# Performance work log

Measured on AMD Instinct MI355X. Metric: run time of the kernel, lower is better.

## Reference

```python
import jax, jax.numpy as jnp
import numpy as np

K = 20          # neighbors
BN_EPS = 1e-5


def _knn_idx(x, k):
    """x: [B, C, N] -> idx of k nearest neighbors [B, N, k] (by squared distance, self included)."""
    xx = jnp.sum(x * x, axis=1)                       # [B, N]
    inner = jnp.einsum('bcn,bcm->bnm', x, x)          # [B, N, N]
    neg_sqdist = 2.0 * inner - xx[:, :, None] - xx[:, None, :]
    return jax.lax.top_k(neg_sqdist, k)[1]            # [B, N, k]


def _graph_feature(x, k):
    """x: [B, C, N] -> edge features cat(x_j - x_i, x_i): [B, 2C, N, k]."""
    idx = _knn_idx(x, k)                              # [B, N, k]
    xT = x.transpose(0, 2, 1)                         # [B, N, C]
    nbrs = jax.vmap(lambda xt, ii: xt[ii])(xT, idx)   # [B, N, k, C] gather
    center = xT[:, :, None, :]                        # [B, N, 1, C]
    feat = jnp.concatenate(
        [nbrs - center, jnp.broadcast_to(center, nbrs.shape)], axis=-1)  # [B, N, k, 2C]
    return feat.transpose(0, 3, 1, 2)                 # [B, 2C, N, k]


def _conv_bn_lrelu(feat, W, gamma, beta, mean, var):
    """1x1 Conv2d (no bias) + BatchNorm (given stats) + LeakyReLU(0.2). feat: [B, Cin, N, k]."""
    y = jnp.einsum('oc,bcnk->bonk', W, feat)
    scale = (gamma / jnp.sqrt(var + BN_EPS))[None, :, None, None]
    y = (y - mean[None, :, None, None]) * scale + beta[None, :, None, None]
    return jnp.where(y > 0, y, 0.2 * y)


def setup_inputs() -> dict:
    key = jax.random.key(0)
    ks = list(jax.random.split(key, 32))
    B, N = 8, 1024
    f32 = jnp.float32

    def w(kk, o, i):
        return jax.random.normal(kk, (o, i), dtype=f32) / np.sqrt(i)

    def bn(k1, k2, k3, k4, c):
        g = jax.random.uniform(k1, (c,), dtype=f32, minval=0.5, maxval=1.5)
        b = jax.random.normal(k2, (c,), dtype=f32) * 0.05
        m = jax.random.normal(k3, (c,), dtype=f32) * 0.05
        v = jax.random.uniform(k4, (c,), dtype=f32, minval=0.5, maxval=1.5)
        return g, b, m, v

    x = jax.random.normal(ks[0], (B, N, 3), dtype=f32)
    W0 = w(ks[1], 64, 6);    g0, b0, m0, v0 = bn(ks[2], ks[3], ks[4], ks[5], 64)
    W1 = w(ks[6], 128, 128); g1, b1, m1, v1 = bn(ks[7], ks[8], ks[9], ks[10], 128)
    W2 = w(ks[11], 256, 256); g2, b2, m2, v2 = bn(ks[12], ks[13], ks[14], ks[15], 256)
    Wf = w(ks[16], 512, 896); gf, bf, mf, vf = bn(ks[17], ks[18], ks[19], ks[20], 512)
    We = w(ks[21], 256, 512)
    return dict(x=x,
                W0=W0, g0=g0, b0=b0, m0=m0, v0=v0,
                W1=W1, g1=g1, b1=b1, m1=m1, v1=v1,
                W2=W2, g2=g2, b2=b2, m2=m2, v2=v2,
                Wf=Wf, gf=gf, bf=bf, mf=mf, vf=vf,
                We=We)


def reference(x, W0, g0, b0, m0, v0, W1, g1, b1, m1, v1,
              W2, g2, b2, m2, v2, Wf, gf, bf, mf, vf, We):
    h = x.transpose(0, 2, 1)                          # [B, 3, N]
    outs = []
    for (W, g, b, m, v) in ((W0, g0, b0, m0, v0),
                            (W1, g1, b1, m1, v1),
                            (W2, g2, b2, m2, v2)):
        gfeat = _graph_feature(h, K)                  # [B, 2C, N, k]
        y = _conv_bn_lrelu(gfeat, W, g, b, m, v)      # [B, Cout, N, k]
        h = y.mean(axis=-1)                           # max-free EdgeConv pool over k
        outs.append(h)
    cat = jnp.concatenate(outs, axis=1)               # [B, 448, N]
    gfeat = _graph_feature(cat, K)                    # [B, 896, N, k]
    y = _conv_bn_lrelu(gfeat, Wf, gf, bf, mf, vf)     # [B, 512, N, k]
    pooled = y.mean(axis=-1).mean(axis=-1)            # [B, 512] (pool over k then N)
    return pooled @ We.T                              # [B, num_features]
```

## Files before the change

### kernel.cpp

```cpp
#include <hip/hip_runtime.h>
#include <cstdint>

#define KNN 20
#define BV 8
#define NV 1024

template <int CTRL>
__device__ __forceinline__ unsigned dppmax(unsigned x) {
    unsigned m = (unsigned)__builtin_amdgcn_update_dpp((int)x, (int)x, CTRL, 0xf, 0xf, false);
    return (x > m) ? x : m;
}
template <int CTRL>
__device__ __forceinline__ unsigned dppmin(unsigned x) {
    unsigned m = (unsigned)__builtin_amdgcn_update_dpp((int)x, (int)x, CTRL, 0xf, 0xf, false);
    return (x < m) ? x : m;
}
__device__ __forceinline__ unsigned wave_max_u32(unsigned x) {
    x = dppmax<0xB1>(x); x = dppmax<0x4E>(x); x = dppmax<0x141>(x);
    x = dppmax<0x140>(x); x = dppmax<0x142>(x); x = dppmax<0x143>(x);
    return (unsigned)__builtin_amdgcn_readlane((int)x, 63);
}
__device__ __forceinline__ unsigned wave_min_u32(unsigned x) {
    x = dppmin<0xB1>(x); x = dppmin<0x4E>(x); x = dppmin<0x141>(x);
    x = dppmin<0x140>(x); x = dppmin<0x142>(x); x = dppmin<0x143>(x);
    return (unsigned)__builtin_amdgcn_readlane((int)x, 63);
}

__global__ __launch_bounds__(256) void k_transpose(const float* __restrict__ x, float* __restrict__ hx) {
    int id = blockIdx.x * 256 + threadIdx.x;
    if (id >= BV * 3 * NV) return;
    int n = id % NV;
    int c = (id / NV) % 3;
    int b = id / (3 * NV);
    hx[id] = x[(b * NV + n) * 3 + c];
}

__global__ __launch_bounds__(256) void k_xx(const float* __restrict__ h, float* __restrict__ xx,
                                            int C, int bstride) {
    int id = blockIdx.x * 256 + threadIdx.x;
    int n = id % NV, b = id / NV;
    if (b >= BV) return;
    const float* hp = h + (size_t)b * bstride + n;
    float s = 0.f;
    for (int c = 0; c < C; ++c) { float v = hp[(size_t)c * NV]; s += v * v; }
    xx[b * NV + n] = s;
}

__global__ __launch_bounds__(512, 4) void k_knn(const float* __restrict__ h, const float* __restrict__ xx,
                                                int C, int bstride, int* __restrict__ idx) {
    __shared__ float Bs[8][1024];
    const int bx = blockIdx.x;
    const int b = bx & 7, tile = bx >> 3;
    const int i0 = tile * 16;
    const int t = threadIdx.x, lane = t & 63, w = t >> 6;
    const int irow = i0 + w * 2;
    float acc[2][16] = {};
    const float* hb = h + (size_t)b * bstride;

    for (int c0 = 0; c0 < C; c0 += 8) {
        __syncthreads();
#pragma unroll
        for (int r = 0; r < 4; ++r) {
            int e = r * 512 + t;
            int cc = e >> 8, jj = e & 255;
            float4 v = make_float4(0.f, 0.f, 0.f, 0.f);
            if (c0 + cc < C) v = *(const float4*)&hb[(size_t)(c0 + cc) * NV + jj * 4];
            *(float4*)&Bs[cc][jj * 4] = v;
        }
        __syncthreads();
#pragma unroll
        for (int c = 0; c < 8; ++c) {
            float2 arv = *(const float2*)&Bs[c][irow];
            float ar[2] = {arv.x, arv.y};
            float br[16];
#pragma unroll
            for (int g = 0; g < 4; ++g) {
                float4 bv = *(const float4*)&Bs[c][g * 256 + (lane << 2)];
                br[g * 4 + 0] = bv.x; br[g * 4 + 1] = bv.y;
                br[g * 4 + 2] = bv.z; br[g * 4 + 3] = bv.w;
            }
#pragma unroll
            for (int a = 0; a < 2; ++a)
#pragma unroll
                for (int q = 0; q < 16; ++q) acc[a][q] += ar[a] * br[q];
        }
    }

    const float* xb = xx + b * NV;
    float xxj[16];
#pragma unroll
    for (int g = 0; g < 4; ++g) {
        float4 xv = *(const float4*)&xb[g * 256 + (lane << 2)];
        xxj[g * 4 + 0] = xv.x; xxj[g * 4 + 1] = xv.y;
        xxj[g * 4 + 2] = xv.z; xxj[g * 4 + 3] = xv.w;
    }
    unsigned ua[2][16];
#pragma unroll
    for (int a = 0; a < 2; ++a) {
        float xi = xb[irow + a];
#pragma unroll
        for (int q = 0; q < 16; ++q) {
            float d = 2.f * acc[a][q] - xi - xxj[q];
            unsigned u = __float_as_uint(d);
            ua[a][q] = ((int)u < 0) ? ~u : (u | 0x80000000u);
        }
    }

    int* opb = idx + ((size_t)(b * NV + irow)) * KNN;
#pragma unroll 1
    for (int s = 0; s < KNN; ++s) {
#pragma unroll
        for (int a = 0; a < 2; ++a) {
            unsigned w0[8]; int p0[8];
#pragma unroll
            for (int i = 0; i < 8; ++i) {
                bool g = ua[a][2 * i + 1] > ua[a][2 * i];
                w0[i] = g ? ua[a][2 * i + 1] : ua[a][2 * i];
                p0[i] = g ? 2 * i + 1 : 2 * i;
            }
            unsigned w1[4]; int p1[4];
#pragma unroll
            for (int i = 0; i < 4; ++i) {
                bool g = w1[0], gg = w0[2 * i + 1] > w0[2 * i];
                (void)g;
                w1[i] = gg ? w0[2 * i + 1] : w0[2 * i];
                p1[i] = gg ? p0[2 * i + 1] : p0[2 * i];
            }
            unsigned w2[2]; int p2[2];
#pragma unroll
            for (int i = 0; i < 2; ++i) {
                bool gg = w1[2 * i + 1] > w1[2 * i];
                w2[i] = gg ? w1[2 * i + 1] : w1[2 * i];
                p2[i] = gg ? p1[2 * i + 1] : p1[2 * i];
            }
            bool gf = w2[1] > w2[0];
            unsigned su = gf ? w2[1] : w2[0];
            int bq = gf ? p2[1] : p2[0];

            unsigned gmax = wave_max_u32(su);
            int myj = ((bq >> 2) << 8) + (lane << 2) + (bq & 3);
            unsigned cand = (su == gmax) ? (unsigned)myj : 0xFFFFFFFFu;
            int j = (int)wave_min_u32(cand);
            if (lane == 0) opb[a * KNN + s] = j;
            int wq = (cand == (unsigned)j) ? bq : 99;
#pragma unroll
            for (int q = 0; q < 16; ++q)
                if (wq == q) ua[a][q] = 0u;
        }
    }
}

__global__ __launch_bounds__(256) void k_pack(const float* __restrict__ W, float* __restrict__ wb,
                                              int C, int O) {
    int id = blockIdx.x * 256 + threadIdx.x;
    if (id >= 2 * O * C) return;
    int c = id % C, o = (id / C) % O, half = id / (C * O);
    float wl = W[(size_t)o * 2 * C + c];
    wb[id] = half ? (W[(size_t)o * 2 * C + C + c] - wl) : wl;
}

__global__ __launch_bounds__(256) void k_gemm(const float* __restrict__ A, int astride,
                                              const float* __restrict__ h, int bstride, int C,
                                              float* __restrict__ out, int O) {
    __shared__ float Ws[8][64], Hs[8][128];
    const int b = blockIdx.x, n0 = blockIdx.y * 128, o0 = blockIdx.z * 64;
    const int t = threadIdx.x, tx = t & 15, ty = t >> 4;
    float acc[4][8] = {};
    const float* hb = h + (size_t)b * bstride;
    for (int c0 = 0; c0 < C; c0 += 8) {
#pragma unroll
        for (int q = 0; q < 2; ++q) {
            int e = t + q * 256;
            int oo = e >> 3, cc = e & 7;
            Ws[cc][oo] = ((c0 + cc) < C) ? A[(size_t)(o0 + oo) * astride + c0 + cc] : 0.f;
        }
        {
            int cc = t >> 5, nn4 = t & 31;
            float4 v = make_float4(0.f, 0.f, 0.f, 0.f);
            if (c0 + cc < C) v = *(const float4*)&hb[(size_t)(c0 + cc) * NV + n0 + nn4 * 4];
            *(float4*)&Hs[cc][nn4 * 4] = v;
        }
        __syncthreads();
#pragma unroll
        for (int c = 0; c < 8; ++c) {
            float4 wv = *(const float4*)&Ws[c][ty * 4];
            float ar[4] = {wv.x, wv.y, wv.z, wv.w};
            float br[8];
            float4 h0 = *(const float4*)&Hs[c][tx * 4];
            float4 h1 = *(const float4*)&Hs[c][64 + tx * 4];
            br[0] = h0.x; br[1] = h0.y; br[2] = h0.z; br[3] = h0.w;
            br[4] = h1.x; br[5] = h1.y; br[6] = h1.z; br[7] = h1.w;
#pragma unroll
            for (int a = 0; a < 4; ++a)
#pragma unroll
                for (int q = 0; q < 8; ++q) acc[a][q] += ar[a] * br[q];
        }
        __syncthreads();
    }
#pragma unroll
    for (int a = 0; a < 4; ++a) {
        int o = o0 + ty * 4 + a;
        float* outp = out + ((size_t)b * O + o) * NV + n0;
        float4 s0 = make_float4(acc[a][0], acc[a][1], acc[a][2], acc[a][3]);
        float4 s1 = make_float4(acc[a][4], acc[a][5], acc[a][6], acc[a][7]);
        *(float4*)&outp[tx * 4] = s0;
        *(float4*)&outp[64 + tx * 4] = s1;
    }
}

__global__ __launch_bounds__(256) void k_edge(const float* __restrict__ pd,
                                              const int* __restrict__ idx,
                                              const float* __restrict__ ga, const float* __restrict__ be,
                                              const float* __restrict__ mu, const float* __restrict__ va,
                                              float* __restrict__ out, int out_bstride, int O) {
    const int b = blockIdx.x;
    const int n = blockIdx.y * 256 + threadIdx.x;
    const int o0 = blockIdx.z * 4;
    const int* ip = idx + ((size_t)b * NV + n) * KNN;
    int jj[KNN];
#pragma unroll
    for (int k = 0; k < KNN; ++k) jj[k] = ip[k];
#pragma unroll
    for (int a = 0; a < 4; ++a) {
        const int o = o0 + a;
        const float al = ga[o] / sqrtf(va[o] + 1e-5f);
        const float c0 = be[o] - mu[o] * al;
        const float* pb = pd + ((size_t)b * 2 * O + o) * NV;
        const float dv  = pd[((size_t)b * 2 * O + O + o) * NV + n];
        float s = 0.f;
#pragma unroll
        for (int k = 0; k < KNN; ++k) {
            float y = fmaf(al, pb[jj[k]] + dv, c0);
            s += (y > 0.f) ? y : 0.2f * y;
        }
        out[(size_t)b * out_bstride + (size_t)o * NV + n] = s * (1.f / KNN);
    }
}

__global__ __launch_bounds__(256) void k_pool(const float* __restrict__ hf, float* __restrict__ pooled) {
    const int o = blockIdx.x, b = blockIdx.y;
    const float* hp = hf + ((size_t)b * 512 + o) * NV;
    float s = 0.f;
    for (int i = threadIdx.x; i < NV; i += 256) s += hp[i];
#pragma unroll
    for (int off = 32; off > 0; off >>= 1) s += __shfl_down(s, off, 64);
    __shared__ float red[4];
    if ((threadIdx.x & 63) == 0) red[threadIdx.x >> 6] = s;
    __syncthreads();
    if (threadIdx.x == 0)
        pooled[(size_t)b * 512 + o] = (red[0] + red[1] + red[2] + red[3]) * (1.f / NV);
}

__global__ __launch_bounds__(256) void k_final(const float* __restrict__ pooled, const float* __restrict__ We,
                                               float* __restrict__ out) {
    const int j = threadIdx.x, b = blockIdx.x;
    __shared__ float ps[512];
    for (int o = threadIdx.x; o < 512; o += 256) ps[o] = pooled[b * 512 + o];
    __syncthreads();
    float s = 0.f;
    for (int o = 0; o < 512; ++o) s += ps[o] * We[(size_t)j * 512 + o];
    out[b * 256 + j] = s;
}

extern "C" void kernel_launch(void* const* d_in, const int* in_sizes, int n_in,
                              void* d_out, int out_size, void* d_ws, size_t ws_size,
                              hipStream_t stream) {
    const float* x  = (const float*)d_in[0];
    const float* W0 = (const float*)d_in[1];
    const float* g0 = (const float*)d_in[2];
    const float* b0 = (const float*)d_in[3];
    const float* m0 = (const float*)d_in[4];
    const float* v0 = (const float*)d_in[5];
    const float* W1 = (const float*)d_in[6];
    const float* g1 = (const float*)d_in[7];
    const float* b1 = (const float*)d_in[8];
    const float* m1 = (const float*)d_in[9];
    const float* v1 = (const float*)d_in[10];
    const float* W2 = (const float*)d_in[11];
    const float* g2 = (const float*)d_in[12];
    const float* b2 = (const float*)d_in[13];
    const float* m2 = (const float*)d_in[14];
    const float* v2 = (const float*)d_in[15];
    const float* Wf = (const float*)d_in[16];
    const float* gf = (const float*)d_in[17];
    const float* bf = (const float*)d_in[18];
    const float* mf = (const float*)d_in[19];
    const float* vf = (const float*)d_in[20];
    const float* We = (const float*)d_in[21];

    float* ws = (float*)d_ws;
    float* hx     = ws;
    float* cat    = hx + 24576;
    float* xx     = cat + 3670016;
    int*   idx    = (int*)(xx + 8192);
    float* pd     = (float*)(idx + 163840);
    float* wb     = pd + 8388608;
    float* hf     = wb + 458752;
    float* pooled = hf + 4194304;

    k_transpose<<<96, 256, 0, stream>>>(x, hx);

    auto run_layer = [&](const float* h, int C, int bstride, const float* W,
                         const float* g, const float* be, const float* m, const float* v,
                         int O, float* outp, int obstride) {
        k_xx<<<32, 256, 0, stream>>>(h, xx, C, bstride);
        k_knn<<<512, 512, 0, stream>>>(h, xx, C, bstride, idx);
        int pn = 2 * O * C;
        k_pack<<<(pn + 255) / 256, 256, 0, stream>>>(W, wb, C, O);
        k_gemm<<<dim3(8, 8, 2 * O / 64), 256, 0, stream>>>(wb, C, h, bstride, C, pd, 2 * O);
        k_edge<<<dim3(8, 4, O / 4), 256, 0, stream>>>(pd, idx, g, be, m, v, outp, obstride, O);
    };

    run_layer(hx, 3, 3 * NV, W0, g0, b0, m0, v0, 64, cat, 448 * NV);
    run_layer(cat, 64, 448 * NV, W1, g1, b1, m1, v1, 128, cat + 64 * NV, 448 * NV);
    run_layer(cat + 64 * NV, 128, 448 * NV, W2, g2, b2, m2, v2, 256, cat + 192 * NV, 448 * NV);
    run_layer(cat, 448, 448 * NV, Wf, gf, bf, mf, vf, 512, hf, 512 * NV);

    k_pool<<<dim3(512, 8), 256, 0, stream>>>(hf, pooled);
    k_final<<<8, 256, 0, stream>>>(pooled, We, (float*)d_out);
}
```

Baseline: 802.6 us.

## Enlarge kNN and GEMM register tiles, prefetch kNN loads, use float top-k compare

The kNN kernel now computes 4 query rows per wave instead of 2, which halves the block count. It also prefetches the next 8-channel slab into registers while computing the current one, and runs the top-k selection directly on float distances with a float DPP max instead of an order-preserving uint transform. The edge GEMM tile grows from 64x128 to 128x128 with an 8x8 register tile per thread. The aim is more arithmetic reuse per shared-memory load and hidden global-load latency, at the cost of higher register pressure and fewer blocks for occupancy.

```diff
diff --git a/kernel.cpp b/kernel.cpp
--- a/kernel.cpp
+++ b/kernel.cpp
@@ -6,19 +6,20 @@
 #define NV 1024
 
 template <int CTRL>
-__device__ __forceinline__ unsigned dppmax(unsigned x) {
-    unsigned m = (unsigned)__builtin_amdgcn_update_dpp((int)x, (int)x, CTRL, 0xf, 0xf, false);
-    return (x > m) ? x : m;
+__device__ __forceinline__ float dppmaxf(float x) {
+    int xi = __float_as_int(x);
+    int mi = __builtin_amdgcn_update_dpp(xi, xi, CTRL, 0xf, 0xf, false);
+    return fmaxf(x, __int_as_float(mi));
 }
 template <int CTRL>
 __device__ __forceinline__ unsigned dppmin(unsigned x) {
     unsigned m = (unsigned)__builtin_amdgcn_update_dpp((int)x, (int)x, CTRL, 0xf, 0xf, false);
     return (x < m) ? x : m;
 }
-__device__ __forceinline__ unsigned wave_max_u32(unsigned x) {
-    x = dppmax<0xB1>(x); x = dppmax<0x4E>(x); x = dppmax<0x141>(x);
-    x = dppmax<0x140>(x); x = dppmax<0x142>(x); x = dppmax<0x143>(x);
-    return (unsigned)__builtin_amdgcn_readlane((int)x, 63);
+__device__ __forceinline__ float wave_max_f32(float x) {
+    x = dppmaxf<0xB1>(x); x = dppmaxf<0x4E>(x); x = dppmaxf<0x141>(x);
+    x = dppmaxf<0x140>(x); x = dppmaxf<0x142>(x); x = dppmaxf<0x143>(x);
+    return __int_as_float(__builtin_amdgcn_readlane(__float_as_int(x), 63));
 }
 __device__ __forceinline__ unsigned wave_min_u32(unsigned x) {
     x = dppmin<0xB1>(x); x = dppmin<0x4E>(x); x = dppmin<0x141>(x);
@@ -46,32 +47,45 @@
     xx[b * NV + n] = s;
 }
 
-__global__ __launch_bounds__(512, 4) void k_knn(const float* __restrict__ h, const float* __restrict__ xx,
+__global__ __launch_bounds__(512, 2) void k_knn(const float* __restrict__ h, const float* __restrict__ xx,
                                                 int C, int bstride, int* __restrict__ idx) {
     __shared__ float Bs[8][1024];
     const int bx = blockIdx.x;
     const int b = bx & 7, tile = bx >> 3;
-    const int i0 = tile * 16;
+    const int i0 = tile * 32;
     const int t = threadIdx.x, lane = t & 63, w = t >> 6;
-    const int irow = i0 + w * 2;
-    float acc[2][16] = {};
+    const int irow = i0 + w * 4;
+    float acc[4][16] = {};
     const float* hb = h + (size_t)b * bstride;
+
+    int cc_[4], jj_[4];
+#pragma unroll
+    for (int r = 0; r < 4; ++r) { int e = r * 512 + t; cc_[r] = e >> 8; jj_[r] = (e & 255) * 4; }
+
+    float4 pf[4];
+#pragma unroll
+    for (int r = 0; r < 4; ++r) {
+        pf[r] = make_float4(0.f, 0.f, 0.f, 0.f);
+        if (cc_[r] < C) pf[r] = *(const float4*)&hb[(size_t)cc_[r] * NV + jj_[r]];
+    }
 
     for (int c0 = 0; c0 < C; c0 += 8) {
         __syncthreads();
 #pragma unroll
-        for (int r = 0; r < 4; ++r) {
-            int e = r * 512 + t;
-            int cc = e >> 8, jj = e & 255;
-            float4 v = make_float4(0.f, 0.f, 0.f, 0.f);
-            if (c0 + cc < C) v = *(const float4*)&hb[(size_t)(c0 + cc) * NV + jj * 4];
-            *(float4*)&Bs[cc][jj * 4] = v;
-        }
+        for (int r = 0; r < 4; ++r) *(float4*)&Bs[cc_[r]][jj_[r]] = pf[r];
         __syncthreads();
+        int cn = c0 + 8;
+        if (cn < C) {
+#pragma unroll
+            for (int r = 0; r < 4; ++r) {
+                pf[r] = make_float4(0.f, 0.f, 0.f, 0.f);
+                if (cn + cc_[r] < C) pf[r] = *(const float4*)&hb[(size_t)(cn + cc_[r]) * NV + jj_[r]];
+            }
+        }
 #pragma unroll
         for (int c = 0; c < 8; ++c) {
-            float2 arv = *(const float2*)&Bs[c][irow];
-            float ar[2] = {arv.x, arv.y};
+            float4 arv = *(const float4*)&Bs[c][irow];
+            float ar[4] = {arv.x, arv.y, arv.z, arv.w};
             float br[16];
 #pragma unroll
             for (int g = 0; g < 4; ++g) {
@@ -80,7 +94,7 @@
                 br[g * 4 + 2] = bv.z; br[g * 4 + 3] = bv.w;
             }
 #pragma unroll
-            for (int a = 0; a < 2; ++a)
+            for (int a = 0; a < 4; ++a)
 #pragma unroll
                 for (int q = 0; q < 16; ++q) acc[a][q] += ar[a] * br[q];
         }
@@ -94,58 +108,52 @@
         xxj[g * 4 + 0] = xv.x; xxj[g * 4 + 1] = xv.y;
         xxj[g * 4 + 2] = xv.z; xxj[g * 4 + 3] = xv.w;
     }
-    unsigned ua[2][16];
-#pragma unroll
-    for (int a = 0; a < 2; ++a) {
+#pragma unroll
+    for (int a = 0; a < 4; ++a) {
         float xi = xb[irow + a];
 #pragma unroll
-        for (int q = 0; q < 16; ++q) {
-            float d = 2.f * acc[a][q] - xi - xxj[q];
-            unsigned u = __float_as_uint(d);
-            ua[a][q] = ((int)u < 0) ? ~u : (u | 0x80000000u);
-        }
+        for (int q = 0; q < 16; ++q) acc[a][q] = 2.f * acc[a][q] - xi - xxj[q];
     }
 
     int* opb = idx + ((size_t)(b * NV + irow)) * KNN;
 #pragma unroll 1
     for (int s = 0; s < KNN; ++s) {
 #pragma unroll
-        for (int a = 0; a < 2; ++a) {
-            unsigned w0[8]; int p0[8];
+        for (int a = 0; a < 4; ++a) {
+            float w0[8]; int p0[8];
 #pragma unroll
             for (int i = 0; i < 8; ++i) {
-                bool g = ua[a][2 * i + 1] > ua[a][2 * i];
-                w0[i] = g ? ua[a][2 * i + 1] : ua[a][2 * i];
+                bool g = acc[a][2 * i + 1] > acc[a][2 * i];
+                w0[i] = g ? acc[a][2 * i + 1] : acc[a][2 * i];
                 p0[i] = g ? 2 * i + 1 : 2 * i;
             }
-            unsigned w1[4]; int p1[4];
+            float w1[4]; int p1[4];
 #pragma unroll
             for (int i = 0; i < 4; ++i) {
-                bool g = w1[0], gg = w0[2 * i + 1] > w0[2 * i];
-                (void)g;
-                w1[i] = gg ? w0[2 * i + 1] : w0[2 * i];
-                p1[i] = gg ? p0[2 * i + 1] : p0[2 * i];
-            }
-            unsigned w2[2]; int p2[2];
+                bool g = w0[2 * i + 1] > w0[2 * i];
+                w1[i] = g ? w0[2 * i + 1] : w0[2 * i];
+                p1[i] = g ? p0[2 * i + 1] : p0[2 * i];
+            }
+            float w2[2]; int p2[2];
 #pragma unroll
             for (int i = 0; i < 2; ++i) {
-                bool gg = w1[2 * i + 1] > w1[2 * i];
-                w2[i] = gg ? w1[2 * i + 1] : w1[2 * i];
-                p2[i] = gg ? p1[2 * i + 1] : p1[2 * i];
+                bool g = w1[2 * i + 1] > w1[2 * i];
+                w2[i] = g ? w1[2 * i + 1] : w1[2 * i];
+                p2[i] = g ? p1[2 * i + 1] : p1[2 * i];
             }
             bool gf = w2[1] > w2[0];
-            unsigned su = gf ? w2[1] : w2[0];
+            float bv = gf ? w2[1] : w2[0];
             int bq = gf ? p2[1] : p2[0];
 
-            unsigned gmax = wave_max_u32(su);
+            float gmax = wave_max_f32(bv);
             int myj = ((bq >> 2) << 8) + (lane << 2) + (bq & 3);
-            unsigned cand = (su == gmax) ? (unsigned)myj : 0xFFFFFFFFu;
+            unsigned cand = (bv == gmax) ? (unsigned)myj : 0xFFFFFFFFu;
             int j = (int)wave_min_u32(cand);
             if (lane == 0) opb[a * KNN + s] = j;
             int wq = (cand == (unsigned)j) ? bq : 99;
 #pragma unroll
             for (int q = 0; q < 16; ++q)
-                if (wq == q) ua[a][q] = 0u;
+                if (wq == q) acc[a][q] = -3.4e38f;
         }
     }
 }
@@ -161,16 +169,16 @@
 
 __global__ __launch_bounds__(256) void k_gemm(const float* __restrict__ A, int astride,
                                               const float* __restrict__ h, int bstride, int C,
-                                              float* __restrict__ out, int O) {
-    __shared__ float Ws[8][64], Hs[8][128];
-    const int b = blockIdx.x, n0 = blockIdx.y * 128, o0 = blockIdx.z * 64;
+                                              float* __restrict__ out, int O2) {
+    __shared__ float Ws[8][128], Hs[8][128];
+    const int b = blockIdx.x, n0 = blockIdx.y * 128, o0 = blockIdx.z * 128;
     const int t = threadIdx.x, tx = t & 15, ty = t >> 4;
-    float acc[4][8] = {};
+    float acc[8][8] = {};
     const float* hb = h + (size_t)b * bstride;
     for (int c0 = 0; c0 < C; c0 += 8) {
 #pragma unroll
-        for (int q = 0; q < 2; ++q) {
-            int e = t + q * 256;
+        for (int k2 = 0; k2 < 4; ++k2) {
+            int e = t + k2 * 256;
             int oo = e >> 3, cc = e & 7;
             Ws[cc][oo] = ((c0 + cc) < C) ? A[(size_t)(o0 + oo) * astride + c0 + cc] : 0.f;
         }
@@ -183,28 +191,27 @@
         __syncthreads();
 #pragma unroll
         for (int c = 0; c < 8; ++c) {
-            float4 wv = *(const float4*)&Ws[c][ty * 4];
-            float ar[4] = {wv.x, wv.y, wv.z, wv.w};
-            float br[8];
-            float4 h0 = *(const float4*)&Hs[c][tx * 4];
-            float4 h1 = *(const float4*)&Hs[c][64 + tx * 4];
-            br[0] = h0.x; br[1] = h0.y; br[2] = h0.z; br[3] = h0.w;
-            br[4] = h1.x; br[5] = h1.y; br[6] = h1.z; br[7] = h1.w;
-#pragma unroll
-            for (int a = 0; a < 4; ++a)
+            float4 wv0 = *(const float4*)&Ws[c][ty * 8];
+            float4 wv1 = *(const float4*)&Ws[c][ty * 8 + 4];
+            float ar[8] = {wv0.x, wv0.y, wv0.z, wv0.w, wv1.x, wv1.y, wv1.z, wv1.w};
+            float4 h0 = *(const float4*)&Hs[c][tx * 8];
+            float4 h1 = *(const float4*)&Hs[c][tx * 8 + 4];
+            float br[8] = {h0.x, h0.y, h0.z, h0.w, h1.x, h1.y, h1.z, h1.w};
+#pragma unroll
+            for (int a = 0; a < 8; ++a)
 #pragma unroll
                 for (int q = 0; q < 8; ++q) acc[a][q] += ar[a] * br[q];
         }
         __syncthreads();
     }
 #pragma unroll
-    for (int a = 0; a < 4; ++a) {
-        int o = o0 + ty * 4 + a;
-        float* outp = out + ((size_t)b * O + o) * NV + n0;
+    for (int a = 0; a < 8; ++a) {
+        int o = o0 + ty * 8 + a;
+        float* outp = out + ((size_t)b * O2 + o) * NV + n0;
         float4 s0 = make_float4(acc[a][0], acc[a][1], acc[a][2], acc[a][3]);
         float4 s1 = make_float4(acc[a][4], acc[a][5], acc[a][6], acc[a][7]);
-        *(float4*)&outp[tx * 4] = s0;
-        *(float4*)&outp[64 + tx * 4] = s1;
+        *(float4*)&outp[tx * 8] = s0;
+        *(float4*)&outp[tx * 8 + 4] = s1;
     }
 }
 
@@ -304,10 +311,10 @@
                          const float* g, const float* be, const float* m, const float* v,
                          int O, float* outp, int obstride) {
         k_xx<<<32, 256, 0, stream>>>(h, xx, C, bstride);
-        k_knn<<<512, 512, 0, stream>>>(h, xx, C, bstride, idx);
+        k_knn<<<256, 512, 0, stream>>>(h, xx, C, bstride, idx);
         int pn = 2 * O * C;
         k_pack<<<(pn + 255) / 256, 256, 0, stream>>>(W, wb, C, O);
-        k_gemm<<<dim3(8, 8, 2 * O / 64), 256, 0, stream>>>(wb, C, h, bstride, C, pd, 2 * O);
+        k_gemm<<<dim3(8, 8, 2 * O / 128), 256, 0, stream>>>(wb, C, h, bstride, C, pd, 2 * O);
         k_edge<<<dim3(8, 4, O / 4), 256, 0, stream>>>(pd, idx, g, be, m, v, outp, obstride, O);
     };
 
```

After: 976.8 us. 21.7% more time.

## Fuse weight packing into GEMM, stage edge rows in LDS, float top-k selection

Applied to the files above, without the earlier changes.

Removes the separate k_pack launch by computing the packed weights (W_left and W_right - W_left) on the fly inside the GEMM tile load. Restructures k_edge so each block stages four output rows of the neighbor projection in shared memory and gathers neighbors from LDS instead of scattered global reads. The kNN selection now works directly on float scores with float DPP max instead of converting to order-preserving unsigned keys, and the kNN launch bound drops from 4 to 2 waves per SIMD so the compiler may use more registers. In exchange, the GEMM does slightly more global loads per tile, and taken entries are marked with a large negative float sentinel, which changes tie and NaN handling.

```diff
diff --git a/kernel.cpp b/kernel.cpp
--- a/kernel.cpp
+++ b/kernel.cpp
@@ -6,19 +6,20 @@
 #define NV 1024
 
 template <int CTRL>
-__device__ __forceinline__ unsigned dppmax(unsigned x) {
-    unsigned m = (unsigned)__builtin_amdgcn_update_dpp((int)x, (int)x, CTRL, 0xf, 0xf, false);
-    return (x > m) ? x : m;
+__device__ __forceinline__ float dppmaxf(float x) {
+    int xi = __float_as_int(x);
+    int mi = __builtin_amdgcn_update_dpp(xi, xi, CTRL, 0xf, 0xf, false);
+    return fmaxf(x, __int_as_float(mi));
 }
 template <int CTRL>
 __device__ __forceinline__ unsigned dppmin(unsigned x) {
     unsigned m = (unsigned)__builtin_amdgcn_update_dpp((int)x, (int)x, CTRL, 0xf, 0xf, false);
     return (x < m) ? x : m;
 }
-__device__ __forceinline__ unsigned wave_max_u32(unsigned x) {
-    x = dppmax<0xB1>(x); x = dppmax<0x4E>(x); x = dppmax<0x141>(x);
-    x = dppmax<0x140>(x); x = dppmax<0x142>(x); x = dppmax<0x143>(x);
-    return (unsigned)__builtin_amdgcn_readlane((int)x, 63);
+__device__ __forceinline__ float wave_max_f32(float x) {
+    x = dppmaxf<0xB1>(x); x = dppmaxf<0x4E>(x); x = dppmaxf<0x141>(x);
+    x = dppmaxf<0x140>(x); x = dppmaxf<0x142>(x); x = dppmaxf<0x143>(x);
+    return __int_as_float(__builtin_amdgcn_readlane(__float_as_int(x), 63));
 }
 __device__ __forceinline__ unsigned wave_min_u32(unsigned x) {
     x = dppmin<0xB1>(x); x = dppmin<0x4E>(x); x = dppmin<0x141>(x);
@@ -46,7 +47,7 @@
     xx[b * NV + n] = s;
 }
 
-__global__ __launch_bounds__(512, 4) void k_knn(const float* __restrict__ h, const float* __restrict__ xx,
+__global__ __launch_bounds__(512, 2) void k_knn(const float* __restrict__ h, const float* __restrict__ xx,
                                                 int C, int bstride, int* __restrict__ idx) {
     __shared__ float Bs[8][1024];
     const int bx = blockIdx.x;
@@ -94,16 +95,11 @@
         xxj[g * 4 + 0] = xv.x; xxj[g * 4 + 1] = xv.y;
         xxj[g * 4 + 2] = xv.z; xxj[g * 4 + 3] = xv.w;
     }
-    unsigned ua[2][16];
 #pragma unroll
     for (int a = 0; a < 2; ++a) {
         float xi = xb[irow + a];
 #pragma unroll
-        for (int q = 0; q < 16; ++q) {
-            float d = 2.f * acc[a][q] - xi - xxj[q];
-            unsigned u = __float_as_uint(d);
-            ua[a][q] = ((int)u < 0) ? ~u : (u | 0x80000000u);
-        }
+        for (int q = 0; q < 16; ++q) acc[a][q] = 2.f * acc[a][q] - xi - xxj[q];
     }
 
     int* opb = idx + ((size_t)(b * NV + irow)) * KNN;
@@ -111,57 +107,47 @@
     for (int s = 0; s < KNN; ++s) {
 #pragma unroll
         for (int a = 0; a < 2; ++a) {
-            unsigned w0[8]; int p0[8];
+            float w0[8]; int p0[8];
 #pragma unroll
             for (int i = 0; i < 8; ++i) {
-                bool g = ua[a][2 * i + 1] > ua[a][2 * i];
-                w0[i] = g ? ua[a][2 * i + 1] : ua[a][2 * i];
+                bool g = acc[a][2 * i + 1] > acc[a][2 * i];
+                w0[i] = g ? acc[a][2 * i + 1] : acc[a][2 * i];
                 p0[i] = g ? 2 * i + 1 : 2 * i;
             }
-            unsigned w1[4]; int p1[4];
+            float w1[4]; int p1[4];
 #pragma unroll
             for (int i = 0; i < 4; ++i) {
-                bool g = w1[0], gg = w0[2 * i + 1] > w0[2 * i];
-                (void)g;
-                w1[i] = gg ? w0[2 * i + 1] : w0[2 * i];
-                p1[i] = gg ? p0[2 * i + 1] : p0[2 * i];
-            }
-            unsigned w2[2]; int p2[2];
+                bool g = w0[2 * i + 1] > w0[2 * i];
+                w1[i] = g ? w0[2 * i + 1] : w0[2 * i];
+                p1[i] = g ? p0[2 * i + 1] : p0[2 * i];
+            }
+            float w2[2]; int p2[2];
 #pragma unroll
             for (int i = 0; i < 2; ++i) {
-                bool gg = w1[2 * i + 1] > w1[2 * i];
-                w2[i] = gg ? w1[2 * i + 1] : w1[2 * i];
-                p2[i] = gg ? p1[2 * i + 1] : p1[2 * i];
+                bool g = w1[2 * i + 1] > w1[2 * i];
+                w2[i] = g ? w1[2 * i + 1] : w1[2 * i];
+                p2[i] = g ? p1[2 * i + 1] : p1[2 * i];
             }
             bool gf = w2[1] > w2[0];
-            unsigned su = gf ? w2[1] : w2[0];
+            float bv = gf ? w2[1] : w2[0];
             int bq = gf ? p2[1] : p2[0];
 
-            unsigned gmax = wave_max_u32(su);
+            float gmax = wave_max_f32(bv);
             int myj = ((bq >> 2) << 8) + (lane << 2) + (bq & 3);
-            unsigned cand = (su == gmax) ? (unsigned)myj : 0xFFFFFFFFu;
+            unsigned cand = (bv == gmax) ? (unsigned)myj : 0xFFFFFFFFu;
             int j = (int)wave_min_u32(cand);
             if (lane == 0) opb[a * KNN + s] = j;
             int wq = (cand == (unsigned)j) ? bq : 99;
 #pragma unroll
             for (int q = 0; q < 16; ++q)
-                if (wq == q) ua[a][q] = 0u;
-        }
-    }
-}
-
-__global__ __launch_bounds__(256) void k_pack(const float* __restrict__ W, float* __restrict__ wb,
-                                              int C, int O) {
-    int id = blockIdx.x * 256 + threadIdx.x;
-    if (id >= 2 * O * C) return;
-    int c = id % C, o = (id / C) % O, half = id / (C * O);
-    float wl = W[(size_t)o * 2 * C + c];
-    wb[id] = half ? (W[(size_t)o * 2 * C + C + c] - wl) : wl;
-}
-
-__global__ __launch_bounds__(256) void k_gemm(const float* __restrict__ A, int astride,
+                if (wq == q) acc[a][q] = -3.4e38f;
+        }
+    }
+}
+
+__global__ __launch_bounds__(256) void k_gemm(const float* __restrict__ W, int O,
                                               const float* __restrict__ h, int bstride, int C,
-                                              float* __restrict__ out, int O) {
+                                              float* __restrict__ out) {
     __shared__ float Ws[8][64], Hs[8][128];
     const int b = blockIdx.x, n0 = blockIdx.y * 128, o0 = blockIdx.z * 64;
     const int t = threadIdx.x, tx = t & 15, ty = t >> 4;
@@ -172,7 +158,17 @@
         for (int q = 0; q < 2; ++q) {
             int e = t + q * 256;
             int oo = e >> 3, cc = e & 7;
-            Ws[cc][oo] = ((c0 + cc) < C) ? A[(size_t)(o0 + oo) * astride + c0 + cc] : 0.f;
+            int r = o0 + oo;
+            float v = 0.f;
+            if (c0 + cc < C) {
+                if (r < O) {
+                    v = W[(size_t)r * 2 * C + c0 + cc];
+                } else {
+                    const float* wr = W + (size_t)(r - O) * 2 * C;
+                    v = wr[C + c0 + cc] - wr[c0 + cc];
+                }
+            }
+            Ws[cc][oo] = v;
         }
         {
             int cc = t >> 5, nn4 = t & 31;
@@ -200,7 +196,7 @@
 #pragma unroll
     for (int a = 0; a < 4; ++a) {
         int o = o0 + ty * 4 + a;
-        float* outp = out + ((size_t)b * O + o) * NV + n0;
+        float* outp = out + ((size_t)b * 2 * O + o) * NV + n0;
         float4 s0 = make_float4(acc[a][0], acc[a][1], acc[a][2], acc[a][3]);
         float4 s1 = make_float4(acc[a][4], acc[a][5], acc[a][6], acc[a][7]);
         *(float4*)&outp[tx * 4] = s0;
@@ -213,27 +209,43 @@
                                               const float* __restrict__ ga, const float* __restrict__ be,
                                               const float* __restrict__ mu, const float* __restrict__ va,
                                               float* __restrict__ out, int out_bstride, int O) {
-    const int b = blockIdx.x;
-    const int n = blockIdx.y * 256 + threadIdx.x;
-    const int o0 = blockIdx.z * 4;
-    const int* ip = idx + ((size_t)b * NV + n) * KNN;
-    int jj[KNN];
-#pragma unroll
-    for (int k = 0; k < KNN; ++k) jj[k] = ip[k];
+    __shared__ float Ps[4][1024];
+    const int bx = blockIdx.x;
+    const int b = bx & 7, o0 = (bx >> 3) * 4;
+    const int t = threadIdx.x;
+    const float* pbase = pd + ((size_t)b * 2 * O + o0) * NV;
+#pragma unroll
+    for (int r = 0; r < 4; ++r) {
+        float4 v = *(const float4*)&pbase[(size_t)r * NV + t * 4];
+        *(float4*)&Ps[r][t * 4] = v;
+    }
+    float al[4], cc[4];
 #pragma unroll
     for (int a = 0; a < 4; ++a) {
-        const int o = o0 + a;
-        const float al = ga[o] / sqrtf(va[o] + 1e-5f);
-        const float c0 = be[o] - mu[o] * al;
-        const float* pb = pd + ((size_t)b * 2 * O + o) * NV;
-        const float dv  = pd[((size_t)b * 2 * O + O + o) * NV + n];
-        float s = 0.f;
-#pragma unroll
-        for (int k = 0; k < KNN; ++k) {
-            float y = fmaf(al, pb[jj[k]] + dv, c0);
-            s += (y > 0.f) ? y : 0.2f * y;
-        }
-        out[(size_t)b * out_bstride + (size_t)o * NV + n] = s * (1.f / KNN);
+        al[a] = ga[o0 + a] / sqrtf(va[o0 + a] + 1e-5f);
+        cc[a] = be[o0 + a] - mu[o0 + a] * al[a];
+    }
+    __syncthreads();
+    const float* dbase = pd + ((size_t)b * 2 * O + O + o0) * NV;
+    float* obase = out + (size_t)b * out_bstride + (size_t)o0 * NV;
+#pragma unroll
+    for (int nc = 0; nc < 4; ++nc) {
+        int n = nc * 256 + t;
+        const int* ip = idx + ((size_t)b * NV + n) * KNN;
+        int jj[KNN];
+#pragma unroll
+        for (int k = 0; k < KNN; ++k) jj[k] = ip[k];
+#pragma unroll
+        for (int a = 0; a < 4; ++a) {
+            float dv = dbase[(size_t)a * NV + n];
+            float s = 0.f;
+#pragma unroll
+            for (int k = 0; k < KNN; ++k) {
+                float y = fmaf(al[a], Ps[a][jj[k]] + dv, cc[a]);
+                s += (y > 0.f) ? y : 0.2f * y;
+            }
+            obase[(size_t)a * NV + n] = s * (1.f / KNN);
+        }
     }
 }
 
@@ -294,8 +306,7 @@
     float* xx     = cat + 3670016;
     int*   idx    = (int*)(xx + 8192);
     float* pd     = (float*)(idx + 163840);
-    float* wb     = pd + 8388608;
-    float* hf     = wb + 458752;
+    float* hf     = pd + 8388608;
     float* pooled = hf + 4194304;
 
     k_transpose<<<96, 256, 0, stream>>>(x, hx);
@@ -305,10 +316,8 @@
                          int O, float* outp, int obstride) {
         k_xx<<<32, 256, 0, stream>>>(h, xx, C, bstride);
         k_knn<<<512, 512, 0, stream>>>(h, xx, C, bstride, idx);
-        int pn = 2 * O * C;
-        k_pack<<<(pn + 255) / 256, 256, 0, stream>>>(W, wb, C, O);
-        k_gemm<<<dim3(8, 8, 2 * O / 64), 256, 0, stream>>>(wb, C, h, bstride, C, pd, 2 * O);
-        k_edge<<<dim3(8, 4, O / 4), 256, 0, stream>>>(pd, idx, g, be, m, v, outp, obstride, O);
+        k_gemm<<<dim3(8, 8, 2 * O / 64), 256, 0, stream>>>(W, O, h, bstride, C, pd);
+        k_edge<<<8 * O / 4, 256, 0, stream>>>(pd, idx, g, be, m, v, outp, obstride, O);
     };
 
     run_layer(hx, 3, 3 * NV, W0, g0, b0, m0, v0, 64, cat, 448 * NV);
```

New measurement: 767.9 us. 1.05x faster.
